# Kernel optimization log

Measured on AMD Instinct MI355X. Metric: run time of the kernel, lower is better.

## Reference

```python
import jax, jax.numpy as jnp
import numpy as np

E, H, FFN, NQ, NL = 1024, 16, 4096, 8, 4
LN_EPS = 1e-5


def _rx(t):
    c = jnp.cos(t / 2).astype(jnp.complex64)
    s = (-1j * jnp.sin(t / 2)).astype(jnp.complex64)
    return jnp.stack([jnp.stack([c, s]), jnp.stack([s, c])])


def _ry(t):
    c = jnp.cos(t / 2).astype(jnp.complex64)
    s = jnp.sin(t / 2).astype(jnp.complex64)
    return jnp.stack([jnp.stack([c, -s]), jnp.stack([s, c])])


def _rz(t):
    tc = t.astype(jnp.complex64)
    e0 = jnp.exp(-1j * tc / 2)
    e1 = jnp.exp(1j * tc / 2)
    z = jnp.zeros((), jnp.complex64)
    return jnp.stack([jnp.stack([e0, z]), jnp.stack([z, e1])])


def _apply_1q(state, gate, q):
    state = jnp.tensordot(gate, state, axes=([1], [q]))
    return jnp.moveaxis(state, 0, q)


def _cnot(state, c, t):
    s0, s1 = jnp.split(state, 2, axis=c)  # each keeps size-1 axis c
    s1 = jnp.flip(s1, axis=t)            # X on target when control=1
    return jnp.concatenate([s0, s1], axis=c)


def quantum_expvals(qparams):
    # statevector sim of the fixed (input-independent) variational circuit
    state = jnp.zeros((2,) * NQ, jnp.complex64).at[(0,) * NQ].set(1.0)
    for l in range(NL):
        for q in range(NQ):
            state = _apply_1q(state, _rx(qparams[l, q, 0]), q)
            state = _apply_1q(state, _ry(qparams[l, q, 1]), q)
            state = _apply_1q(state, _rz(qparams[l, q, 2]), q)
        for i in range(NQ - 1):
            state = _cnot(state, i, i + 1)
        state = _cnot(state, NQ - 1, 0)
    probs = jnp.abs(state) ** 2
    evs = [1.0 - 2.0 * jnp.sum(jnp.take(probs, 1, axis=q)) for q in range(NQ)]
    return jnp.stack(evs).astype(jnp.float32)  # [NQ]


def _layernorm(x, g, b):
    m = jnp.mean(x, axis=-1, keepdims=True)
    v = jnp.mean((x - m) ** 2, axis=-1, keepdims=True)
    return (x - m) / jnp.sqrt(v + LN_EPS) * g + b


def setup_inputs() -> dict:
    key = jax.random.key(0)
    ks = jax.random.split(key, 16)
    s = 1.0 / np.sqrt(E)
    inp = {
        "x": jax.random.normal(ks[0], (4, 1024, E), jnp.float32),
        "Wq": jax.random.normal(ks[1], (E, E), jnp.float32) * s,
        "Wk": jax.random.normal(ks[2], (E, E), jnp.float32) * s,
        "Wv": jax.random.normal(ks[3], (E, E), jnp.float32) * s,
        "Wo": jax.random.normal(ks[4], (E, E), jnp.float32) * s,
        "bo": jnp.zeros((E,), jnp.float32),
        "gate": jnp.ones((H,), jnp.float32),
        "g1": jnp.ones((E,), jnp.float32),
        "b1": jnp.zeros((E,), jnp.float32),
        "g2": jnp.ones((E,), jnp.float32),
        "b2": jnp.zeros((E,), jnp.float32),
        "Wi": jax.random.normal(ks[5], (NQ, E), jnp.float32) * s,
        "bi": jnp.zeros((NQ,), jnp.float32),
        "qparams": jax.random.normal(ks[6], (NL, NQ, 3), jnp.float32),
        "W1": jax.random.normal(ks[7], (FFN, NQ), jnp.float32) / np.sqrt(NQ),
        "bf1": jnp.zeros((FFN,), jnp.float32),
        "W2": jax.random.normal(ks[8], (E, FFN), jnp.float32) / np.sqrt(FFN),
        "bf2": jnp.zeros((E,), jnp.float32),
    }
    return inp


def reference(x, Wq, Wk, Wv, Wo, bo, gate, g1, b1, g2, b2, Wi, bi, qparams, W1, bf1, W2, bf2):
    B, T, _ = x.shape
    d_k = E // H
    # gated multi-head attention (dropout = identity / eval mode)
    q = (x @ Wq.T).reshape(B, T, H, d_k)
    k = (x @ Wk.T).reshape(B, T, H, d_k)
    v = (x @ Wv.T).reshape(B, T, H, d_k)
    scores = jnp.einsum("bqhd,bkhd->bhqk", q, k) / np.sqrt(d_k)
    attn = jax.nn.softmax(scores, axis=-1)
    out = jnp.einsum("bhqk,bkhd->bqhd", attn, v)
    out = out * jax.nn.sigmoid(gate)[None, None, :, None]
    attn_out = out.reshape(B, T, E) @ Wo.T + bo
    h = _layernorm(x + attn_out, g1, b1)
    # quantum FFN: input_linear output is computed but unused by the circuit
    h2d = h.reshape(B * T, E)
    _x_qubits = h2d @ Wi.T + bi  # faithfully computed, unused (as in original)
    evs = quantum_expvals(qparams)                      # [NQ], token-independent
    qout = jnp.broadcast_to(evs, (B * T, NQ))
    f = jax.nn.relu(qout @ W1.T + bf1) @ W2.T + bf2     # [B*T, E]
    ffn_out = f.reshape(B, T, E)
    return _layernorm(h + ffn_out, g2, b2)
```

## Files before the change

### kernel.cpp

```cpp
#include <hip/hip_runtime.h>

#define E_DIM 1024
#define SEQ 1024
#define BATCH 4
#define NHEAD 16
#define DK 64
#define TOK 4096
#define FFN_DIM 4096
#define NQB 8
#define NLAY 4

typedef __attribute__((ext_vector_type(8))) short short8;
typedef __attribute__((ext_vector_type(4))) float f32x4;
typedef unsigned short u16;
typedef unsigned int u32;

__device__ __forceinline__ u16 f2bf(float f) {
  union { float f; unsigned u; } v; v.f = f;
  unsigned r = v.u + 0x7fffu + ((v.u >> 16) & 1u);
  return (u16)(r >> 16);
}

__device__ __forceinline__ u32 cvtpk_bf16(float lo, float hi) {
  u32 r;
  asm("v_cvt_pk_bf16_f32 %0, %1, %2" : "=v"(r) : "v"(lo), "v"(hi));
  return r;
}

__device__ __forceinline__ void gload_lds16(const u16* g, u16* l) {
  __builtin_amdgcn_global_load_lds((const __attribute__((address_space(1))) unsigned int*)g,
                                   (__attribute__((address_space(3))) unsigned int*)l, 16, 0, 0);
}

__global__ void cast_kernel(const float* __restrict__ in, u16* __restrict__ out, int n4) {
  int i = blockIdx.x * blockDim.x + threadIdx.x;
  int stride = gridDim.x * blockDim.x;
  for (; i < n4; i += stride) {
    float4 v = ((const float4*)in)[i];
    ushort4 o;
    o.x = f2bf(v.x); o.y = f2bf(v.y); o.z = f2bf(v.z); o.w = f2bf(v.w);
    ((ushort4*)out)[i] = o;
  }
}

__global__ void cast4_kernel(const float* __restrict__ a0, const float* __restrict__ a1,
                             const float* __restrict__ a2, const float* __restrict__ a3,
                             u16* __restrict__ out, int n4per) {
  const float* src = blockIdx.z == 0 ? a0 : blockIdx.z == 1 ? a1 : blockIdx.z == 2 ? a2 : a3;
  u16* dst = out + (size_t)blockIdx.z * n4per * 4;
  int i = blockIdx.x * blockDim.x + threadIdx.x;
  int stride = gridDim.x * blockDim.x;
  for (; i < n4per; i += stride) {
    float4 v = ((const float4*)src)[i];
    ushort4 o;
    o.x = f2bf(v.x); o.y = f2bf(v.y); o.z = f2bf(v.z); o.w = f2bf(v.w);
    ((ushort4*)dst)[i] = o;
  }
}

template<int F32OUT, int ZTRANS>
__global__ __launch_bounds__(256) void gemm_bt(
    const u16* __restrict__ A,
    const u16* __restrict__ B0, const u16* __restrict__ B1, const u16* __restrict__ B2,
    void* __restrict__ C0, void* __restrict__ C1, void* __restrict__ C2,
    const float* __restrict__ bias, int K, int N) {
  const u16* B = blockIdx.z == 0 ? B0 : blockIdx.z == 1 ? B1 : B2;
  void* C = blockIdx.z == 0 ? C0 : blockIdx.z == 1 ? C1 : C2;
  __shared__ u16 As[128 * 32];
  __shared__ u16 Bs[128 * 32];
  const int tid = threadIdx.x;
  const int lane = tid & 63;
  const int wid = tid >> 6;
  const int wr = wid >> 1, wc = wid & 1;
  const int lr = lane & 15, lg = lane >> 4;
  const int row0 = blockIdx.y * 128;
  const int col0 = blockIdx.x * 128;
  const int ar = tid >> 2;
  const int ak = (tid & 3) * 8;
  const u16* Ag = A + (size_t)(row0 + ar) * K + ak;
  const u16* Bg = B + (size_t)(col0 + ar) * K + ak;
  u16* AsW = &As[wid * 512];
  u16* BsW = &Bs[wid * 512];
  f32x4 acc[4][4];
  const f32x4 fzero = {0.f, 0.f, 0.f, 0.f};
#pragma unroll
  for (int m = 0; m < 4; ++m)
#pragma unroll
    for (int n = 0; n < 4; ++n) acc[m][n] = fzero;
  for (int k0 = 0; k0 < K; k0 += 32) {
    __syncthreads();
    gload_lds16(Ag + k0, AsW);
    gload_lds16(Ag + (size_t)64 * K + k0, AsW + 2048);
    gload_lds16(Bg + k0, BsW);
    gload_lds16(Bg + (size_t)64 * K + k0, BsW + 2048);
    __syncthreads();
    short8 af[4], bfr[4];
#pragma unroll
    for (int m = 0; m < 4; ++m) af[m] = *(const short8*)&As[(wr * 64 + m * 16 + lr) * 32 + lg * 8];
#pragma unroll
    for (int n = 0; n < 4; ++n) bfr[n] = *(const short8*)&Bs[(wc * 64 + n * 16 + lr) * 32 + lg * 8];
#pragma unroll
    for (int m = 0; m < 4; ++m)
#pragma unroll
      for (int n = 0; n < 4; ++n)
        acc[m][n] = __builtin_amdgcn_mfma_f32_16x16x32_bf16(af[m], bfr[n], acc[m][n], 0, 0, 0);
  }
#pragma unroll
  for (int m = 0; m < 4; ++m) {
    const int growb = row0 + wr * 64 + m * 16 + lg * 4;
#pragma unroll
    for (int n = 0; n < 4; ++n) {
      const int gcol = col0 + wc * 64 + n * 16 + lr;
      if (ZTRANS >= 0 && blockIdx.z == ZTRANS) {
        ushort4 t4;
        t4.x = f2bf(acc[m][n][0]); t4.y = f2bf(acc[m][n][1]);
        t4.z = f2bf(acc[m][n][2]); t4.w = f2bf(acc[m][n][3]);
        *(ushort4*)&((u16*)C)[(size_t)gcol * TOK + growb] = t4;
      } else {
#pragma unroll
        for (int r = 0; r < 4; ++r) {
          size_t idx = (size_t)(growb + r) * N + gcol;
          if (F32OUT) ((float*)C)[idx] = acc[m][n][r] + bias[gcol];
          else ((u16*)C)[idx] = f2bf(acc[m][n][r]);
        }
      }
    }
  }
}

__global__ __launch_bounds__(256) void attn_kernel(
    const u16* __restrict__ qb, const u16* __restrict__ kb, const u16* __restrict__ vtb,
    const float* __restrict__ gate, u16* __restrict__ ob) {
  const int bid = blockIdx.x + (blockIdx.y << 4) + (blockIdx.z << 8);
  const int swz = (bid & 7) * 128 + (bid >> 3);
  const int qblk = swz & 15, h = (swz >> 4) & 15, b = swz >> 8;
  const int tid = threadIdx.x, lane = tid & 63, w = tid >> 6;
  const int lr = lane & 15, lg = lane >> 4;
  __shared__ u16 Kl[2][64 * 64];
  __shared__ u16 Vl[2][64 * 64];
  const u16* Qp = qb + (size_t)(b * SEQ + qblk * 64 + w * 16 + lr) * E_DIM + h * DK;
  const short8 bq0 = *(const short8*)&Qp[lg * 8];
  const short8 bq1 = *(const short8*)&Qp[32 + lg * 8];
  const int r0 = tid >> 3;
  const int cs = (tid & 7) ^ (r0 & 7);
  const u16* Kg0 = kb + (size_t)(b * SEQ + r0) * E_DIM + h * DK + cs * 8;
  const u16* Kg1 = Kg0 + (size_t)32 * E_DIM;
  const u16* Vg0 = vtb + (size_t)(h * DK + r0) * TOK + b * SEQ + cs * 8;
  const u16* Vg1 = Vg0 + (size_t)32 * TOK;
  const int ldsb = w * 512;
#define STAGE(bufi, kt) do { \
    const size_t ko = (size_t)(kt) * 64 * E_DIM; const int vo = (kt) * 64; \
    gload_lds16(Kg0 + ko, &Kl[bufi][ldsb]); \
    gload_lds16(Kg1 + ko, &Kl[bufi][2048 + ldsb]); \
    gload_lds16(Vg0 + vo, &Vl[bufi][ldsb]); \
    gload_lds16(Vg1 + vo, &Vl[bufi][2048 + ldsb]); \
  } while (0)
  f32x4 o[4];
  const f32x4 fzero = {0.f, 0.f, 0.f, 0.f};
#pragma unroll
  for (int dn = 0; dn < 4; ++dn) o[dn] = fzero;
  float mrun = -1e30f, lrun = 0.f;
  const int sw = (lr & 7) << 3;
  const int srcA = ((lg & 1) << 5) + lr;
  const bool hi = (lg & 2) != 0;
  STAGE(0, 0);
  __syncthreads();
  int cur = 0;
  for (int kt = 0; kt < 16; ++kt) {
    if (kt < 15) STAGE(cur ^ 1, kt + 1);
    const u16* Kc = Kl[cur];
    const u16* Vc = Vl[cur];
    f32x4 sT[4];
#pragma unroll
    for (int n = 0; n < 4; ++n) {
      const int base = (n * 16 + lr) * 64;
      const short8 ka0 = *(const short8*)&Kc[base + ((lg << 3) ^ sw)];
      const short8 ka1 = *(const short8*)&Kc[base + ((32 + (lg << 3)) ^ sw)];
      sT[n] = __builtin_amdgcn_mfma_f32_16x16x32_bf16(ka0, bq0, fzero, 0, 0, 0);
      sT[n] = __builtin_amdgcn_mfma_f32_16x16x32_bf16(ka1, bq1, sT[n], 0, 0, 0);
    }
    float mt = sT[0][0];
#pragma unroll
    for (int n = 0; n < 4; ++n)
#pragma unroll
      for (int r = 0; r < 4; ++r) mt = fmaxf(mt, sT[n][r]);
    mt = fmaxf(mt, __shfl_xor(mt, 16));
    mt = fmaxf(mt, __shfl_xor(mt, 32));
    const float mn = fmaxf(mrun, mt * 0.125f);
    const float alpha = __expf(mrun - mn);
    mrun = mn;
    float tsum = 0.f;
    u32 pk[4][2];
#pragma unroll
    for (int n = 0; n < 4; ++n) {
      const float p0 = __expf(sT[n][0] * 0.125f - mn);
      const float p1 = __expf(sT[n][1] * 0.125f - mn);
      const float p2 = __expf(sT[n][2] * 0.125f - mn);
      const float p3 = __expf(sT[n][3] * 0.125f - mn);
      tsum += (p0 + p1) + (p2 + p3);
      pk[n][0] = cvtpk_bf16(p0, p1);
      pk[n][1] = cvtpk_bf16(p2, p3);
    }
    tsum += __shfl_xor(tsum, 16);
    tsum += __shfl_xor(tsum, 32);
    lrun = lrun * alpha + tsum;
#pragma unroll
    for (int dn = 0; dn < 4; ++dn)
#pragma unroll
      for (int r = 0; r < 4; ++r) o[dn][r] *= alpha;
#pragma unroll
    for (int kh = 0; kh < 2; ++kh) {
      const int nb = kh * 2;
      union { short8 s8; u32 d[4]; } pf;
      const u32 a0 = (u32)__shfl((int)pk[nb][0], srcA);
      const u32 c0 = (u32)__shfl((int)pk[nb + 1][0], srcA);
      const u32 a1 = (u32)__shfl((int)pk[nb][1], srcA);
      const u32 c1 = (u32)__shfl((int)pk[nb + 1][1], srcA);
      const u32 a2 = (u32)__shfl((int)pk[nb][0], srcA + 16);
      const u32 c2 = (u32)__shfl((int)pk[nb + 1][0], srcA + 16);
      const u32 a3 = (u32)__shfl((int)pk[nb][1], srcA + 16);
      const u32 c3 = (u32)__shfl((int)pk[nb + 1][1], srcA + 16);
      pf.d[0] = hi ? c0 : a0;
      pf.d[1] = hi ? c1 : a1;
      pf.d[2] = hi ? c2 : a2;
      pf.d[3] = hi ? c3 : a3;
#pragma unroll
      for (int dn = 0; dn < 4; ++dn) {
        const int base = (dn * 16 + lr) * 64;
        const short8 va = *(const short8*)&Vc[base + ((((kh * 4 + lg) << 3)) ^ sw)];
        o[dn] = __builtin_amdgcn_mfma_f32_16x16x32_bf16(va, pf.s8, o[dn], 0, 0, 0);
      }
    }
    __syncthreads();
    cur ^= 1;
  }
  const float sg = 1.f / (1.f + __expf(-gate[h]));
  const float inv = sg / lrun;
  const size_t orow = (size_t)(b * SEQ + qblk * 64 + w * 16 + lr) * E_DIM + h * DK;
#pragma unroll
  for (int dn = 0; dn < 4; ++dn) {
    ushort4 o4;
    o4.x = f2bf(o[dn][0] * inv);
    o4.y = f2bf(o[dn][1] * inv);
    o4.z = f2bf(o[dn][2] * inv);
    o4.w = f2bf(o[dn][3] * inv);
    *(ushort4*)&ob[orow + dn * 16 + lg * 4] = o4;
  }
#undef STAGE
}

__device__ __forceinline__ float2 cmul(float2 a, float2 b) {
  return make_float2(a.x * b.x - a.y * b.y, a.x * b.y + a.y * b.x);
}

__global__ __launch_bounds__(256) void quantum_kernel(
    const float* __restrict__ qparams, const float* __restrict__ W1,
    const float* __restrict__ bf1, float* __restrict__ relu_out) {
  __shared__ float2 st[256];
  __shared__ float pr[256];
  __shared__ float evs_s[NQB];
  const int t = threadIdx.x;
  st[t] = make_float2(t == 0 ? 1.f : 0.f, 0.f);
  for (int l = 0; l < NLAY; ++l) {
    for (int q = 0; q < NQB; ++q) {
      const int stride = 128 >> q;
      for (int g = 0; g < 3; ++g) {
        const float th = qparams[(l * NQB + q) * 3 + g] * 0.5f;
        const float c = cosf(th), sn = sinf(th);
        float2 g00, g01, g10, g11;
        if (g == 0)      { g00 = make_float2(c, 0.f); g01 = make_float2(0.f, -sn); g10 = g01; g11 = g00; }
        else if (g == 1) { g00 = make_float2(c, 0.f); g01 = make_float2(-sn, 0.f); g10 = make_float2(sn, 0.f); g11 = g00; }
        else             { g00 = make_float2(c, -sn); g01 = make_float2(0.f, 0.f); g10 = g01; g11 = make_float2(c, sn); }
        __syncthreads();
        if (t < 128) {
          const int low = t & (stride - 1);
          const int high = t >> (7 - q);
          const int i0 = (high << (8 - q)) | low;
          const int i1 = i0 + stride;
          const float2 a0 = st[i0], a1 = st[i1];
          float2 n0 = cmul(g00, a0), tmp = cmul(g01, a1);
          n0.x += tmp.x; n0.y += tmp.y;
          float2 n1 = cmul(g10, a0); tmp = cmul(g11, a1);
          n1.x += tmp.x; n1.y += tmp.y;
          st[i0] = n0; st[i1] = n1;
        }
      }
    }
    for (int ci = 0; ci < NQB; ++ci) {
      const int cb = 128 >> ci;
      const int tb = 128 >> ((ci + 1) & 7);
      __syncthreads();
      if ((t & cb) && !(t & tb)) {
        const float2 a = st[t];
        const float2 bb = st[t ^ tb];
        st[t] = bb; st[t ^ tb] = a;
      }
    }
  }
  __syncthreads();
  pr[t] = st[t].x * st[t].x + st[t].y * st[t].y;
  __syncthreads();
  if (t < NQB) {
    const int bit = 128 >> t;
    float s = 0.f;
    for (int i = 0; i < 256; ++i)
      if (i & bit) s += pr[i];
    evs_s[t] = 1.f - 2.f * s;
  }
  __syncthreads();
  for (int j = t; j < FFN_DIM; j += 256) {
    float a = bf1[j];
#pragma unroll
    for (int n = 0; n < NQB; ++n) a += evs_s[n] * W1[j * NQB + n];
    relu_out[j] = fmaxf(a, 0.f);
  }
}

__global__ __launch_bounds__(256) void fvec_kernel(
    const float* __restrict__ W2, const float* __restrict__ bf2,
    const float* __restrict__ relu_vec, float* __restrict__ fvec) {
  const int w = threadIdx.x >> 6, lane = threadIdx.x & 63;
  const int e = blockIdx.x * 4 + w;
  const float* row = W2 + (size_t)e * FFN_DIM;
  float s = 0.f;
  for (int i = lane * 4; i < FFN_DIM; i += 256) {
    const float4 wv = *(const float4*)&row[i];
    const float4 rv = *(const float4*)&relu_vec[i];
    s += wv.x * rv.x + wv.y * rv.y + wv.z * rv.z + wv.w * rv.w;
  }
#pragma unroll
  for (int d = 32; d >= 1; d >>= 1) s += __shfl_down(s, d);
  if (lane == 0) fvec[e] = s + bf2[e];
}

__global__ __launch_bounds__(256) void final_ln_kernel(
    const float* __restrict__ x, const float* __restrict__ ao, const float* __restrict__ fvec,
    const float* __restrict__ g1, const float* __restrict__ b1,
    const float* __restrict__ g2, const float* __restrict__ b2, float* __restrict__ out) {
  __shared__ float sm1[8];
  __shared__ float sm2[8];
  const size_t row = blockIdx.x;
  const int tid = threadIdx.x;
  const int w = tid >> 6, lane = tid & 63;
  const float4 xv = *(const float4*)&x[row * E_DIM + tid * 4];
  const float4 av = *(const float4*)&ao[row * E_DIM + tid * 4];
  float v0 = xv.x + av.x, v1 = xv.y + av.y, v2 = xv.z + av.z, v3 = xv.w + av.w;
  float s = v0 + v1 + v2 + v3;
  float ss = v0 * v0 + v1 * v1 + v2 * v2 + v3 * v3;
#pragma unroll
  for (int d = 32; d >= 1; d >>= 1) { s += __shfl_down(s, d); ss += __shfl_down(ss, d); }
  if (lane == 0) { sm1[w * 2] = s; sm1[w * 2 + 1] = ss; }
  __syncthreads();
  s = sm1[0] + sm1[2] + sm1[4] + sm1[6];
  ss = sm1[1] + sm1[3] + sm1[5] + sm1[7];
  const float mean = s * (1.f / 1024.f);
  const float var = ss * (1.f / 1024.f) - mean * mean;
  const float rstd = rsqrtf(var + 1e-5f);
  const float4 g1v = *(const float4*)&g1[tid * 4];
  const float4 b1v = *(const float4*)&b1[tid * 4];
  const float4 fv = *(const float4*)&fvec[tid * 4];
  float z0 = (v0 - mean) * rstd * g1v.x + b1v.x + fv.x;
  float z1 = (v1 - mean) * rstd * g1v.y + b1v.y + fv.y;
  float z2 = (v2 - mean) * rstd * g1v.z + b1v.z + fv.z;
  float z3 = (v3 - mean) * rstd * g1v.w + b1v.w + fv.w;
  float s2 = z0 + z1 + z2 + z3;
  float ss2 = z0 * z0 + z1 * z1 + z2 * z2 + z3 * z3;
#pragma unroll
  for (int d = 32; d >= 1; d >>= 1) { s2 += __shfl_down(s2, d); ss2 += __shfl_down(ss2, d); }
  if (lane == 0) { sm2[w * 2] = s2; sm2[w * 2 + 1] = ss2; }
  __syncthreads();
  s2 = sm2[0] + sm2[2] + sm2[4] + sm2[6];
  ss2 = sm2[1] + sm2[3] + sm2[5] + sm2[7];
  const float mean2 = s2 * (1.f / 1024.f);
  const float var2 = ss2 * (1.f / 1024.f) - mean2 * mean2;
  const float rstd2 = rsqrtf(var2 + 1e-5f);
  const float4 g2v = *(const float4*)&g2[tid * 4];
  const float4 b2v = *(const float4*)&b2[tid * 4];
  float4 ov;
  ov.x = (z0 - mean2) * rstd2 * g2v.x + b2v.x;
  ov.y = (z1 - mean2) * rstd2 * g2v.y + b2v.y;
  ov.z = (z2 - mean2) * rstd2 * g2v.z + b2v.z;
  ov.w = (z3 - mean2) * rstd2 * g2v.w + b2v.w;
  *(float4*)&out[row * E_DIM + tid * 4] = ov;
}

extern "C" void kernel_launch(void* const* d_in, const int* in_sizes, int n_in,
                              void* d_out, int out_size, void* d_ws, size_t ws_size,
                              hipStream_t stream) {
  (void)in_sizes; (void)n_in; (void)out_size; (void)ws_size;
  const float* x       = (const float*)d_in[0];
  const float* Wq      = (const float*)d_in[1];
  const float* Wk      = (const float*)d_in[2];
  const float* Wv      = (const float*)d_in[3];
  const float* Wo      = (const float*)d_in[4];
  const float* bo      = (const float*)d_in[5];
  const float* gate    = (const float*)d_in[6];
  const float* g1      = (const float*)d_in[7];
  const float* b1      = (const float*)d_in[8];
  const float* g2      = (const float*)d_in[9];
  const float* b2      = (const float*)d_in[10];
  const float* qparams = (const float*)d_in[13];
  const float* W1      = (const float*)d_in[14];
  const float* bf1     = (const float*)d_in[15];
  const float* W2      = (const float*)d_in[16];
  const float* bf2     = (const float*)d_in[17];

  char* ws = (char*)d_ws;
  u16* xb        = (u16*)(ws + 0);
  u16* wqb       = (u16*)(ws + 8388608);
  u16* wkb       = (u16*)(ws + 10485760);
  u16* wvb       = (u16*)(ws + 12582912);
  u16* wob       = (u16*)(ws + 14680064);
  u16* qb        = (u16*)(ws + 16777216);
  u16* kb        = (u16*)(ws + 25165824);
  u16* vtb       = (u16*)(ws + 33554432);
  u16* ab        = (u16*)(ws + 41943040);
  float* ao      = (float*)(ws + 50331648);
  float* relu_vec= (float*)(ws + 67108864);
  float* fvec    = (float*)(ws + 67125248);

  cast_kernel<<<2048, 256, 0, stream>>>(x, xb, TOK * E_DIM / 4);
  cast4_kernel<<<dim3(1024, 1, 4), 256, 0, stream>>>(Wq, Wk, Wv, Wo, wqb, E_DIM * E_DIM / 4);
  quantum_kernel<<<1, 256, 0, stream>>>(qparams, W1, bf1, relu_vec);
  fvec_kernel<<<256, 256, 0, stream>>>(W2, bf2, relu_vec, fvec);
  gemm_bt<0, 2><<<dim3(8, 32, 3), 256, 0, stream>>>(xb, wqb, wkb, wvb, qb, kb, vtb, nullptr, E_DIM, E_DIM);
  attn_kernel<<<dim3(16, 16, 4), 256, 0, stream>>>(qb, kb, vtb, gate, ab);
  gemm_bt<1, -1><<<dim3(8, 32, 1), 256, 0, stream>>>(ab, wob, wob, wob, ao, ao, ao, bo, E_DIM, E_DIM);
  final_ln_kernel<<<4096, 256, 0, stream>>>(x, ao, fvec, g1, b1, g2, b2, (float*)d_out);
}
```

Before: 297.7 us.

## Simulate quantum circuit in registers with wave shuffles instead of LDS barriers

Rewrites the statevector simulation so a single 64-lane wavefront holds all 256 amplitudes in registers (4 per lane) and applies gates and CNOTs through xor shuffles and register swaps. This removes the many __syncthreads barriers and LDS round trips of the old one-gate-per-barrier loop. Expectation values are reduced with a butterfly shuffle, and the W1 projection uses float4 loads. The explicit amplitude mapping is error-prone, and the kernel is a small serial part of the total runtime.

```diff
diff --git a/kernel.cpp b/kernel.cpp
--- a/kernel.cpp
+++ b/kernel.cpp
@@ -249,70 +249,142 @@
 #undef STAGE
 }
 
-__device__ __forceinline__ float2 cmul(float2 a, float2 b) {
-  return make_float2(a.x * b.x - a.y * b.y, a.x * b.y + a.y * b.x);
-}
-
 __global__ __launch_bounds__(256) void quantum_kernel(
     const float* __restrict__ qparams, const float* __restrict__ W1,
     const float* __restrict__ bf1, float* __restrict__ relu_out) {
-  __shared__ float2 st[256];
-  __shared__ float pr[256];
+  __shared__ float csl[96], snl[96];
   __shared__ float evs_s[NQB];
   const int t = threadIdx.x;
-  st[t] = make_float2(t == 0 ? 1.f : 0.f, 0.f);
-  for (int l = 0; l < NLAY; ++l) {
-    for (int q = 0; q < NQB; ++q) {
-      const int stride = 128 >> q;
-      for (int g = 0; g < 3; ++g) {
-        const float th = qparams[(l * NQB + q) * 3 + g] * 0.5f;
-        const float c = cosf(th), sn = sinf(th);
-        float2 g00, g01, g10, g11;
-        if (g == 0)      { g00 = make_float2(c, 0.f); g01 = make_float2(0.f, -sn); g10 = g01; g11 = g00; }
-        else if (g == 1) { g00 = make_float2(c, 0.f); g01 = make_float2(-sn, 0.f); g10 = make_float2(sn, 0.f); g11 = g00; }
-        else             { g00 = make_float2(c, -sn); g01 = make_float2(0.f, 0.f); g10 = g01; g11 = make_float2(c, sn); }
-        __syncthreads();
-        if (t < 128) {
-          const int low = t & (stride - 1);
-          const int high = t >> (7 - q);
-          const int i0 = (high << (8 - q)) | low;
-          const int i1 = i0 + stride;
-          const float2 a0 = st[i0], a1 = st[i1];
-          float2 n0 = cmul(g00, a0), tmp = cmul(g01, a1);
-          n0.x += tmp.x; n0.y += tmp.y;
-          float2 n1 = cmul(g10, a0); tmp = cmul(g11, a1);
-          n1.x += tmp.x; n1.y += tmp.y;
-          st[i0] = n0; st[i1] = n1;
+  if (t < NLAY * NQB * 3) {
+    const float th = qparams[t] * 0.5f;
+    csl[t] = cosf(th);
+    snl[t] = sinf(th);
+  }
+  __syncthreads();
+  if (t < 64) {
+    const int lane = t;
+    float2 a[4];
+    a[0] = make_float2(lane == 0 ? 1.f : 0.f, 0.f);
+    a[1] = make_float2(0.f, 0.f);
+    a[2] = make_float2(0.f, 0.f);
+    a[3] = make_float2(0.f, 0.f);
+#pragma unroll
+    for (int l = 0; l < NLAY; ++l) {
+#pragma unroll
+      for (int q = 0; q < NQB; ++q) {
+        const int pi = (l * NQB + q) * 3;
+        const float cx = csl[pi],     sx = snl[pi];
+        const float cy = csl[pi + 1], sy = snl[pi + 1];
+        const float cz = csl[pi + 2], sz = snl[pi + 2];
+        if (q < 6) {
+          const int m = 1 << (5 - q);
+          const int b = (lane >> (5 - q)) & 1;
+#pragma unroll
+          for (int r = 0; r < 4; ++r) {
+            const float px = __shfl_xor(a[r].x, m);
+            const float py = __shfl_xor(a[r].y, m);
+            a[r] = make_float2(cx * a[r].x + sx * py, cx * a[r].y - sx * px);
+          }
+          const float sgy = b ? sy : -sy;
+#pragma unroll
+          for (int r = 0; r < 4; ++r) {
+            const float px = __shfl_xor(a[r].x, m);
+            const float py = __shfl_xor(a[r].y, m);
+            a[r] = make_float2(cy * a[r].x + sgy * px, cy * a[r].y + sgy * py);
+          }
+          const float sgz = b ? -sz : sz;
+#pragma unroll
+          for (int r = 0; r < 4; ++r)
+            a[r] = make_float2(cz * a[r].x + sgz * a[r].y, cz * a[r].y - sgz * a[r].x);
+        } else if (q == 6) {
+#pragma unroll
+          for (int r = 0; r < 2; ++r) {
+            float2 lo = a[r], hiv = a[r + 2];
+            a[r]     = make_float2(cx * lo.x + sx * hiv.y, cx * lo.y - sx * hiv.x);
+            a[r + 2] = make_float2(cx * hiv.x + sx * lo.y, cx * hiv.y - sx * lo.x);
+          }
+#pragma unroll
+          for (int r = 0; r < 2; ++r) {
+            float2 lo = a[r], hiv = a[r + 2];
+            a[r]     = make_float2(cy * lo.x - sy * hiv.x, cy * lo.y - sy * hiv.y);
+            a[r + 2] = make_float2(sy * lo.x + cy * hiv.x, sy * lo.y + cy * hiv.y);
+          }
+#pragma unroll
+          for (int r = 0; r < 2; ++r) {
+            float2 lo = a[r], hiv = a[r + 2];
+            a[r]     = make_float2(cz * lo.x + sz * lo.y, cz * lo.y - sz * lo.x);
+            a[r + 2] = make_float2(cz * hiv.x - sz * hiv.y, cz * hiv.y + sz * hiv.x);
+          }
+        } else {
+#pragma unroll
+          for (int r = 0; r < 4; r += 2) {
+            float2 lo = a[r], hiv = a[r + 1];
+            a[r]     = make_float2(cx * lo.x + sx * hiv.y, cx * lo.y - sx * hiv.x);
+            a[r + 1] = make_float2(cx * hiv.x + sx * lo.y, cx * hiv.y - sx * lo.x);
+          }
+#pragma unroll
+          for (int r = 0; r < 4; r += 2) {
+            float2 lo = a[r], hiv = a[r + 1];
+            a[r]     = make_float2(cy * lo.x - sy * hiv.x, cy * lo.y - sy * hiv.y);
+            a[r + 1] = make_float2(sy * lo.x + cy * hiv.x, sy * lo.y + cy * hiv.y);
+          }
+#pragma unroll
+          for (int r = 0; r < 4; r += 2) {
+            float2 lo = a[r], hiv = a[r + 1];
+            a[r]     = make_float2(cz * lo.x + sz * lo.y, cz * lo.y - sz * lo.x);
+            a[r + 1] = make_float2(cz * hiv.x - sz * hiv.y, cz * hiv.y + sz * hiv.x);
+          }
         }
       }
+#pragma unroll
+      for (int i = 0; i < 5; ++i) {
+        const int cbit = 5 - i;
+        const int tmask = 1 << (4 - i);
+        const int ctrl = (lane >> cbit) & 1;
+#pragma unroll
+        for (int r = 0; r < 4; ++r) {
+          const float px = __shfl_xor(a[r].x, tmask);
+          const float py = __shfl_xor(a[r].y, tmask);
+          if (ctrl) a[r] = make_float2(px, py);
+        }
+      }
+      if (lane & 1) {
+        float2 t0 = a[0]; a[0] = a[2]; a[2] = t0;
+        float2 t1 = a[1]; a[1] = a[3]; a[3] = t1;
+      }
+      { float2 tt = a[2]; a[2] = a[3]; a[3] = tt; }
+      a[1].x = __shfl_xor(a[1].x, 32); a[1].y = __shfl_xor(a[1].y, 32);
+      a[3].x = __shfl_xor(a[3].x, 32); a[3].y = __shfl_xor(a[3].y, 32);
     }
-    for (int ci = 0; ci < NQB; ++ci) {
-      const int cb = 128 >> ci;
-      const int tb = 128 >> ((ci + 1) & 7);
-      __syncthreads();
-      if ((t & cb) && !(t & tb)) {
-        const float2 a = st[t];
-        const float2 bb = st[t ^ tb];
-        st[t] = bb; st[t ^ tb] = a;
-      }
+    const float p0 = a[0].x * a[0].x + a[0].y * a[0].y;
+    const float p1 = a[1].x * a[1].x + a[1].y * a[1].y;
+    const float p2 = a[2].x * a[2].x + a[2].y * a[2].y;
+    const float p3 = a[3].x * a[3].x + a[3].y * a[3].y;
+    const float ptot = (p0 + p1) + (p2 + p3);
+    float ev[8];
+#pragma unroll
+    for (int q = 0; q < 6; ++q) ev[q] = ((lane >> (5 - q)) & 1) ? ptot : 0.f;
+    ev[6] = p2 + p3;
+    ev[7] = p1 + p3;
+#pragma unroll
+    for (int d = 1; d < 64; d <<= 1)
+#pragma unroll
+      for (int q = 0; q < 8; ++q) ev[q] += __shfl_xor(ev[q], d);
+    if (lane == 0) {
+#pragma unroll
+      for (int q = 0; q < 8; ++q) evs_s[q] = 1.f - 2.f * ev[q];
     }
   }
   __syncthreads();
-  pr[t] = st[t].x * st[t].x + st[t].y * st[t].y;
-  __syncthreads();
-  if (t < NQB) {
-    const int bit = 128 >> t;
-    float s = 0.f;
-    for (int i = 0; i < 256; ++i)
-      if (i & bit) s += pr[i];
-    evs_s[t] = 1.f - 2.f * s;
-  }
-  __syncthreads();
+  float e0 = evs_s[0], e1 = evs_s[1], e2 = evs_s[2], e3 = evs_s[3];
+  float e4 = evs_s[4], e5 = evs_s[5], e6 = evs_s[6], e7 = evs_s[7];
   for (int j = t; j < FFN_DIM; j += 256) {
-    float a = bf1[j];
-#pragma unroll
-    for (int n = 0; n < NQB; ++n) a += evs_s[n] * W1[j * NQB + n];
-    relu_out[j] = fmaxf(a, 0.f);
+    const float4 w0 = *(const float4*)&W1[j * NQB];
+    const float4 w1 = *(const float4*)&W1[j * NQB + 4];
+    float acc = bf1[j];
+    acc += e0 * w0.x + e1 * w0.y + e2 * w0.z + e3 * w0.w;
+    acc += e4 * w1.x + e5 * w1.y + e6 * w1.z + e7 * w1.w;
+    relu_out[j] = fmaxf(acc, 0.f);
   }
 }
 
```

After: 253.0 us. 1.18x faster.
